# Performance work log

Hardware: AMD Instinct MI355X
Metric: run time of the kernel (lower is better)

The kernel has to match this reference:

```python
import jax, jax.numpy as jnp
from jax import lax
import numpy as np

POOL = 4
STRIDE = 2


def _window_sum(x, k, s):
    # x: [B,H,W,1] -> sliding-window sum over kxk spatial windows, VALID padding
    return lax.reduce_window(x, jnp.float32(0.0), lax.add,
                             window_dimensions=(1, k, k, 1),
                             window_strides=(1, s, s, 1),
                             padding='VALID')


def setup_inputs() -> dict:
    key = jax.random.key(0)
    x = jax.random.normal(key, (64, 1024, 1024, 1), dtype=jnp.float32)
    return {"input_data": x}


def reference(input_data) -> jnp.ndarray:
    # Equivalent to: extract_patches(kxk, stride s, VALID) -> reduce_std over each window.
    # Computed without materializing patches: std = sqrt(E[x^2] - E[x]^2) per window.
    k, s = POOL, STRIDE
    n = jnp.float32(k * k)
    wsum = _window_sum(input_data, k, s)            # [B,Ho,Wo,1]
    wsumsq = _window_sum(input_data * input_data, k, s)
    mean = wsum / n
    var = jnp.maximum(wsumsq / n - mean * mean, 0.0)
    std = jnp.sqrt(var)                              # [B,Ho,Wo,1]
    b, ho, wo, _ = std.shape
    return std.reshape(b, ho * wo)                   # matches (B, H_out*W_out)
```

## Files before the change

### kernel.cpp

```cpp
#include <hip/hip_runtime.h>


#define IN_H 1024
#define IN_W 1024
#define OUT_H 511
#define OUT_W 511
#define STRIPS 32
#define ROWS_PER_STRIP 16

__global__ __launch_bounds__(256, 8) void stdpool_kernel(
    const float* __restrict__ in, float* __restrict__ out) {
  const int tid = threadIdx.x;
  const int w = tid >> 6;
  const int l = tid & 63;
  const int strip = blockIdx.x;
  const int b = blockIdx.y;

  const int col0 = w * 256 + l * 4;
  const int o0 = w * 128 + l * 2;
  const bool has_o1 = (o0 + 1) < OUT_W;
  const bool tail = (l == 63) && has_o1;

  const int j0 = strip * ROWS_PER_STRIP;
  const int jn = min(ROWS_PER_STRIP, OUT_H - j0);
  const int t0 = j0, t1 = j0 + jn;

  const float* __restrict__ src = in + (size_t)b * IN_H * IN_W;
  float* __restrict__ dst = out + (size_t)b * OUT_H * OUT_W;

  const float* rp = src + (size_t)(2 * t0) * IN_W + col0;
  float4 a = *(const float4*)rp;
  float4 c = *(const float4*)(rp + IN_W);

  float Pp0 = 0.f, Pp1 = 0.f, Qp0 = 0.f, Qp1 = 0.f;

  for (int t = t0; t <= t1; ++t) {
    float4 na = make_float4(0.f, 0.f, 0.f, 0.f);
    float4 nc = na;
    if (t < t1) {
      const float* np = src + (size_t)(2 * (t + 1)) * IN_W + col0;
      na = *(const float4*)np;
      nc = *(const float4*)(np + IN_W);
    }

    float c0 = (a.x + a.y) + (c.x + c.y);
    float c1 = (a.z + a.w) + (c.z + c.w);
    float d0 = fmaf(a.y, a.y, a.x * a.x) + fmaf(c.y, c.y, c.x * c.x);
    float d1 = fmaf(a.w, a.w, a.z * a.z) + fmaf(c.w, c.w, c.z * c.z);

    float cn = __shfl_down(c0, 1, 64);
    float dn = __shfl_down(d0, 1, 64);
    if (tail) {
      const float* tp = src + (size_t)(2 * t) * IN_W + col0 + 4;
      const float2 e0 = *(const float2*)tp;
      const float2 e1 = *(const float2*)(tp + IN_W);
      cn = (e0.x + e0.y) + (e1.x + e1.y);
      dn = fmaf(e0.y, e0.y, e0.x * e0.x) + fmaf(e1.y, e1.y, e1.x * e1.x);
    }

    const float P0 = c0 + c1, P1 = c1 + cn;
    const float Q0 = d0 + d1, Q1 = d1 + dn;

    if (t > t0) {
      const float inv = 1.0f / 16.0f;
      const float s0 = Pp0 + P0, s1 = Pp1 + P1;
      const float q0 = Qp0 + Q0, q1 = Qp1 + Q1;
      const float m0 = s0 * inv, m1 = s1 * inv;
      const float v0 = fmaxf(fmaf(-m0, m0, q0 * inv), 0.0f);
      const float v1 = fmaxf(fmaf(-m1, m1, q1 * inv), 0.0f);
      float* op = dst + (size_t)(t - 1) * OUT_W + o0;
      op[0] = sqrtf(v0);
      if (has_o1) op[1] = sqrtf(v1);
    }

    Pp0 = P0; Pp1 = P1; Qp0 = Q0; Qp1 = Q1;
    a = na; c = nc;
  }
}

extern "C" void kernel_launch(void* const* d_in, const int* in_sizes, int n_in,
                              void* d_out, int out_size, void* d_ws,
                              size_t ws_size, hipStream_t stream) {
  const float* x = (const float*)d_in[0];
  float* out = (float*)d_out;

  dim3 block(256, 1, 1);
  dim3 grid(STRIPS, 64, 1);
  stdpool_kernel<<<grid, block, 0, stream>>>(x, out);
}
```

Before: 393.8 us.

## Fully unroll row loop with two-deep prefetch and doubled strip height

After: 380.5 us. -3.4%, faster.

```diff
diff --git a/kernel.cpp b/kernel.cpp
--- a/kernel.cpp
+++ b/kernel.cpp
@@ -5,10 +5,11 @@
 #define IN_W 1024
 #define OUT_H 511
 #define OUT_W 511
-#define STRIPS 32
-#define ROWS_PER_STRIP 16
+#define STRIPS 16
+#define ORPS 32
+#define PAIRS (ORPS + 1)
 
-__global__ __launch_bounds__(256, 8) void stdpool_kernel(
+__global__ __launch_bounds__(256, 4) void stdpool_kernel(
     const float* __restrict__ in, float* __restrict__ out) {
   const int tid = threadIdx.x;
   const int w = tid >> 6;
@@ -21,60 +22,76 @@
   const bool has_o1 = (o0 + 1) < OUT_W;
   const bool tail = (l == 63) && has_o1;
 
-  const int j0 = strip * ROWS_PER_STRIP;
-  const int jn = min(ROWS_PER_STRIP, OUT_H - j0);
-  const int t0 = j0, t1 = j0 + jn;
+  const int t0 = strip * ORPS;
 
-  const float* __restrict__ src = in + (size_t)b * IN_H * IN_W;
-  float* __restrict__ dst = out + (size_t)b * OUT_H * OUT_W;
+  const float* __restrict__ src = in + (size_t)b * IN_H * IN_W + col0;
+  float* __restrict__ dst = out + (size_t)b * OUT_H * OUT_W + o0;
 
-  const float* rp = src + (size_t)(2 * t0) * IN_W + col0;
-  float4 a = *(const float4*)rp;
-  float4 c = *(const float4*)(rp + IN_W);
+  float4 A[2], C[2];
+  float2 E0[2], E1[2];
+
+#pragma unroll
+  for (int t = 0; t < 2; ++t) {
+    const float* p = src + (size_t)(2 * (t0 + t)) * IN_W;
+    A[t] = *(const float4*)p;
+    C[t] = *(const float4*)(p + IN_W);
+    if (tail) {
+      E0[t] = *(const float2*)(p + 4);
+      E1[t] = *(const float2*)(p + IN_W + 4);
+    }
+  }
 
   float Pp0 = 0.f, Pp1 = 0.f, Qp0 = 0.f, Qp1 = 0.f;
 
-  for (int t = t0; t <= t1; ++t) {
-    float4 na = make_float4(0.f, 0.f, 0.f, 0.f);
-    float4 nc = na;
-    if (t < t1) {
-      const float* np = src + (size_t)(2 * (t + 1)) * IN_W + col0;
-      na = *(const float4*)np;
-      nc = *(const float4*)(np + IN_W);
+#pragma unroll
+  for (int t = 0; t < PAIRS; ++t) {
+    const int k = t & 1;
+    const float4 a = A[k], c = C[k];
+    const float2 e0 = E0[k], e1 = E1[k];
+
+    if (t + 2 < PAIRS) {
+      int r = 2 * (t0 + t + 2);
+      if (r > IN_H - 2) r = IN_H - 2;
+      const float* p = src + (size_t)r * IN_W;
+      A[k] = *(const float4*)p;
+      C[k] = *(const float4*)(p + IN_W);
+      if (tail) {
+        E0[k] = *(const float2*)(p + 4);
+        E1[k] = *(const float2*)(p + IN_W + 4);
+      }
     }
 
-    float c0 = (a.x + a.y) + (c.x + c.y);
-    float c1 = (a.z + a.w) + (c.z + c.w);
-    float d0 = fmaf(a.y, a.y, a.x * a.x) + fmaf(c.y, c.y, c.x * c.x);
-    float d1 = fmaf(a.w, a.w, a.z * a.z) + fmaf(c.w, c.w, c.z * c.z);
+    const float c0 = (a.x + a.y) + (c.x + c.y);
+    const float c1 = (a.z + a.w) + (c.z + c.w);
+    const float d0 = fmaf(a.x, a.x, a.y * a.y) + fmaf(c.x, c.x, c.y * c.y);
+    const float d1 = fmaf(a.z, a.z, a.w * a.w) + fmaf(c.z, c.z, c.w * c.w);
 
     float cn = __shfl_down(c0, 1, 64);
     float dn = __shfl_down(d0, 1, 64);
     if (tail) {
-      const float* tp = src + (size_t)(2 * t) * IN_W + col0 + 4;
-      const float2 e0 = *(const float2*)tp;
-      const float2 e1 = *(const float2*)(tp + IN_W);
       cn = (e0.x + e0.y) + (e1.x + e1.y);
-      dn = fmaf(e0.y, e0.y, e0.x * e0.x) + fmaf(e1.y, e1.y, e1.x * e1.x);
+      dn = fmaf(e0.x, e0.x, e0.y * e0.y) + fmaf(e1.x, e1.x, e1.y * e1.y);
     }
 
     const float P0 = c0 + c1, P1 = c1 + cn;
     const float Q0 = d0 + d1, Q1 = d1 + dn;
 
-    if (t > t0) {
-      const float inv = 1.0f / 16.0f;
-      const float s0 = Pp0 + P0, s1 = Pp1 + P1;
-      const float q0 = Qp0 + Q0, q1 = Qp1 + Q1;
-      const float m0 = s0 * inv, m1 = s1 * inv;
-      const float v0 = fmaxf(fmaf(-m0, m0, q0 * inv), 0.0f);
-      const float v1 = fmaxf(fmaf(-m1, m1, q1 * inv), 0.0f);
-      float* op = dst + (size_t)(t - 1) * OUT_W + o0;
-      op[0] = sqrtf(v0);
-      if (has_o1) op[1] = sqrtf(v1);
+    if (t > 0) {
+      const int orow = t0 + t - 1;
+      if (orow < OUT_H) {
+        const float inv = 1.0f / 16.0f;
+        const float s0 = Pp0 + P0, s1 = Pp1 + P1;
+        const float q0 = Qp0 + Q0, q1 = Qp1 + Q1;
+        const float m0 = s0 * inv, m1 = s1 * inv;
+        const float v0 = fmaxf(fmaf(-m0, m0, q0 * inv), 0.0f);
+        const float v1 = fmaxf(fmaf(-m1, m1, q1 * inv), 0.0f);
+        float* op = dst + (size_t)orow * OUT_W;
+        op[0] = sqrtf(v0);
+        if (has_o1) op[1] = sqrtf(v1);
+      }
     }
 
     Pp0 = P0; Pp1 = P1; Qp0 = Q0; Qp1 = Q1;
-    a = na; c = nc;
   }
 }
 
```
